# Kernel tuning notes

Measured on AMD Instinct MI355X. Metric: run time of the kernel, lower is better.

## Reference

```python
import jax, jax.numpy as jnp
import numpy as np

NUM_HEADS = 2

def mha(q, k, v, w_in, b_in, w_out, b_out):
    # torch nn.MultiheadAttention with batch_first=True, packed in_proj
    E = q.shape[-1]
    Dh = E // NUM_HEADS
    wq, wk, wv = jnp.split(w_in, 3, axis=0)
    bq, bk, bv = jnp.split(b_in, 3, axis=0)
    qh = (q @ wq.T + bq).reshape(q.shape[0], q.shape[1], NUM_HEADS, Dh)
    kh = (k @ wk.T + bk).reshape(k.shape[0], k.shape[1], NUM_HEADS, Dh)
    vh = (v @ wv.T + bv).reshape(v.shape[0], v.shape[1], NUM_HEADS, Dh)
    scores = jnp.einsum('blhd,bmhd->bhlm', qh, kh) / jnp.sqrt(jnp.asarray(Dh, q.dtype))
    attn = jax.nn.softmax(scores, axis=-1)
    ctx = jnp.einsum('bhlm,bmhd->blhd', attn, vh).reshape(q.shape[0], q.shape[1], E)
    return ctx @ w_out.T + b_out


def setup_inputs() -> dict:
    key = jax.random.key(0)
    ks = jax.random.split(key, 10)
    B, S, F, E, H = 16384, 512, 4, 8, 16
    s = 0.3
    return {
        'x': jax.random.normal(ks[0], (B, S, E), jnp.float32),
        'Q': jax.random.normal(ks[1], (F, E), jnp.float32) * s,
        'sa_w_in': jax.random.normal(ks[2], (3 * E, E), jnp.float32) * s,
        'sa_b_in': jnp.zeros((3 * E,), jnp.float32),
        'sa_w_out': jax.random.normal(ks[3], (E, E), jnp.float32) * s,
        'sa_b_out': jnp.zeros((E,), jnp.float32),
        'ca_w_in': jax.random.normal(ks[4], (3 * E, E), jnp.float32) * s,
        'ca_b_in': jnp.zeros((3 * E,), jnp.float32),
        'ca_w_out': jax.random.normal(ks[5], (E, E), jnp.float32) * s,
        'ca_b_out': jnp.zeros((E,), jnp.float32),
        'r_w1': jax.random.normal(ks[6], (H, F * E), jnp.float32) * s,
        'r_b1': jnp.zeros((H,), jnp.float32),
        'r_w2': jax.random.normal(ks[7], (1, H), jnp.float32) * s,
        'r_b2': jnp.zeros((1,), jnp.float32),
    }


def reference(x, Q, sa_w_in, sa_b_in, sa_w_out, sa_b_out,
              ca_w_in, ca_b_in, ca_w_out, ca_b_out,
              r_w1, r_b1, r_w2, r_b2):
    B = x.shape[0]
    # self-attention over the (batch-identical) factor queries
    Qb = jnp.broadcast_to(Q[None], (B,) + Q.shape)  # [B, F, E]
    Q_upd = mha(Qb, Qb, Qb, sa_w_in, sa_b_in, sa_w_out, sa_b_out)
    # cross-attention: factors attend over the input sequence
    Q_cross = mha(Q_upd, x, x, ca_w_in, ca_b_in, ca_w_out, ca_b_out)  # [B, F, E]
    similarity = jnp.einsum('bfe,bse->bfs', Q_cross, x)  # [B, F, S]
    attn_weights = jax.nn.softmax(similarity, axis=-1)
    final_factors = jnp.einsum('bfs,bse->bfe', attn_weights, x)  # [B, F, E]
    fused = final_factors.reshape(B, -1)  # [B, F*E]
    h = jax.nn.relu(fused @ r_w1.T + r_b1)
    out = h @ r_w2.T + r_b2  # [B, 1]
    return out, similarity
```

## Files before the change

kernel.cpp:

```cpp
#include <hip/hip_runtime.h>

#define SEQ 512
#define EMB 8
#define NFAC 4

typedef float v2f __attribute__((ext_vector_type(2)));

__device__ __forceinline__ float rfl(float v) {
    return __int_as_float(__builtin_amdgcn_readfirstlane(__float_as_int(v)));
}

__global__ void precompute_kernel(
    const float* __restrict__ Q,
    const float* __restrict__ sa_w_in, const float* __restrict__ sa_b_in,
    const float* __restrict__ sa_w_out, const float* __restrict__ sa_b_out,
    const float* __restrict__ ca_w_in, const float* __restrict__ ca_b_in,
    const float* __restrict__ ca_w_out, const float* __restrict__ ca_b_out,
    float* __restrict__ ws)
{
    const int t = threadIdx.x;
    __shared__ float sw[608];
    __shared__ float sqh[32], skh[32], svh[32], sctx[32], sQu[32], sqc[32];
    enum { OQ = 0, SWIN = 32, SBIN = 224, SWOUT = 248, SBOUT = 312,
           CWIN = 320, CBIN = 512, CWOUT = 536, CBOUT = 600 };

    for (int i = t; i < 32;  i += 64) sw[OQ + i]    = Q[i];
    for (int i = t; i < 192; i += 64) sw[SWIN + i]  = sa_w_in[i];
    for (int i = t; i < 24;  i += 64) sw[SBIN + i]  = sa_b_in[i];
    for (int i = t; i < 64;  i += 64) sw[SWOUT + i] = sa_w_out[i];
    if (t < 8) sw[SBOUT + t] = sa_b_out[t];
    for (int i = t; i < 192; i += 64) sw[CWIN + i]  = ca_w_in[i];
    for (int i = t; i < 24;  i += 64) sw[CBIN + i]  = ca_b_in[i];
    for (int i = t; i < 64;  i += 64) sw[CWOUT + i] = ca_w_out[i];
    if (t < 8) sw[CBOUT + t] = ca_b_out[t];
    __syncthreads();

    {
        const int e2 = t >> 3, e = t & 7;
        float m0 = 0.f, m1 = 0.f;
        #pragma unroll
        for (int d = 0; d < 4; ++d) {
            m0 += sw[CWOUT + e2 * 8 + d]     * sw[CWIN + (16 + d) * 8 + e];
            m1 += sw[CWOUT + e2 * 8 + 4 + d] * sw[CWIN + (20 + d) * 8 + e];
        }
        ws[72 + t]  = m0;
        ws[136 + t] = m1;
    }
    if (t < 8) {
        float a = sw[CBOUT + t];
        #pragma unroll
        for (int d = 0; d < 8; ++d) a += sw[CWOUT + t * 8 + d] * sw[CBIN + 16 + d];
        ws[200 + t] = a;
    }

    if (t < 32) {
        const int l = t >> 3, j = t & 7;
        float aq = sw[SBIN + j], ak = sw[SBIN + 8 + j], av = sw[SBIN + 16 + j];
        #pragma unroll
        for (int e = 0; e < 8; ++e) {
            const float q = sw[OQ + l * 8 + e];
            aq += q * sw[SWIN + j * 8 + e];
            ak += q * sw[SWIN + (8 + j) * 8 + e];
            av += q * sw[SWIN + (16 + j) * 8 + e];
        }
        sqh[t] = aq; skh[t] = ak; svh[t] = av;
    }
    __syncthreads();

    if (t < 8) {
        const int h = t >> 2, l = t & 3;
        float sc[4], mx = -1e30f;
        #pragma unroll
        for (int m = 0; m < 4; ++m) {
            float a = 0.f;
            #pragma unroll
            for (int d = 0; d < 4; ++d) a += sqh[l * 8 + h * 4 + d] * skh[m * 8 + h * 4 + d];
            sc[m] = 0.5f * a;
            mx = fmaxf(mx, sc[m]);
        }
        float ssum = 0.f;
        #pragma unroll
        for (int m = 0; m < 4; ++m) { sc[m] = __expf(sc[m] - mx); ssum += sc[m]; }
        const float inv = 1.f / ssum;
        #pragma unroll
        for (int d = 0; d < 4; ++d) {
            float a = 0.f;
            #pragma unroll
            for (int m = 0; m < 4; ++m) a += sc[m] * svh[m * 8 + h * 4 + d];
            sctx[l * 8 + h * 4 + d] = a * inv;
        }
    }
    __syncthreads();

    if (t < 32) {
        const int l = t >> 3, e2 = t & 7;
        float a = sw[SBOUT + e2];
        #pragma unroll
        for (int e = 0; e < 8; ++e) a += sctx[l * 8 + e] * sw[SWOUT + e2 * 8 + e];
        sQu[l * 8 + e2] = a;
    }
    __syncthreads();

    if (t < 32) {
        const int l = t >> 3, j = t & 7;
        float a = sw[CBIN + j];
        #pragma unroll
        for (int e = 0; e < 8; ++e) a += sQu[l * 8 + e] * sw[CWIN + j * 8 + e];
        sqc[l * 8 + j] = a;
    }
    __syncthreads();

    {
        const int p = t >> 3, e = t & 7, h = p >> 2, f = p & 3;
        float a = 0.f;
        #pragma unroll
        for (int d = 0; d < 4; ++d)
            a += sqc[f * 8 + h * 4 + d] * sw[CWIN + (8 + h * 4 + d) * 8 + e];
        ws[p * 8 + e] = 0.5f * a;
    }
    if (t < 8) {
        const int p = t, h = p >> 2, f = p & 3;
        float a = 0.f;
        #pragma unroll
        for (int d = 0; d < 4; ++d) a += sqc[f * 8 + h * 4 + d] * sw[CBIN + 8 + h * 4 + d];
        ws[64 + p] = 0.5f * a;
    }
}

__global__ __launch_bounds__(256, 4) void fused_kernel(
    const float* __restrict__ x,
    const float* __restrict__ r_w1, const float* __restrict__ r_b1,
    const float* __restrict__ r_w2, const float* __restrict__ r_b2,
    const float* __restrict__ ws,
    float* __restrict__ out, float* __restrict__ sim_out)
{
    const int b = blockIdx.x;
    const int tid = threadIdx.x;
    const int w = __builtin_amdgcn_readfirstlane(tid >> 6);
    const int lane = tid & 63;
    const int c7 = lane & 7;

    __shared__ float su[64];
    __shared__ float sff[32];

    const float* xb = x + (size_t)b * (SEQ * EMB);

    const int p0 = 2 * w, p1 = 2 * w + 1;
    v2f wq0[4], wq1[4];
    #pragma unroll
    for (int i = 0; i < 4; ++i) {
        wq0[i] = v2f{rfl(ws[p0 * 8 + 2 * i]), rfl(ws[p0 * 8 + 2 * i + 1])};
        wq1[i] = v2f{rfl(ws[p1 * 8 + 2 * i]), rfl(ws[p1 * 8 + 2 * i + 1])};
    }
    const float cb0 = rfl(ws[64 + p0]), cb1 = rfl(ws[64 + p1]);

    float4 L0[8], L1[8];
    #pragma unroll
    for (int j = 0; j < 8; ++j) {
        const float4* xp = (const float4*)(xb + (lane + 64 * j) * 8);
        L0[j] = xp[0];
        L1[j] = xp[1];
    }

    v2f xa0[4] = {}, xa1[4] = {};
    float sum0 = 0.f, sum1 = 0.f;
    #pragma unroll
    for (int j = 0; j < 8; ++j) {
        v2f xv[4];
        xv[0] = v2f{L0[j].x, L0[j].y}; xv[1] = v2f{L0[j].z, L0[j].w};
        xv[2] = v2f{L1[j].x, L1[j].y}; xv[3] = v2f{L1[j].z, L1[j].w};
        v2f s0 = {cb0, 0.f}, s1 = {cb1, 0.f};
        #pragma unroll
        for (int i = 0; i < 4; ++i) { s0 += wq0[i] * xv[i]; s1 += wq1[i] * xv[i]; }
        const float e0 = __expf(s0.x + s0.y), e1 = __expf(s1.x + s1.y);
        sum0 += e0; sum1 += e1;
        #pragma unroll
        for (int i = 0; i < 4; ++i) { xa0[i] += e0 * xv[i]; xa1[i] += e1 * xv[i]; }
    }
    float* a0 = (float*)xa0;
    float* a1 = (float*)xa1;
    #pragma unroll
    for (int m = 1; m < 8; m <<= 1) {
        sum0 += __shfl_xor(sum0, m, 64);
        sum1 += __shfl_xor(sum1, m, 64);
        #pragma unroll
        for (int e = 0; e < 8; ++e) {
            a0[e] += __shfl_xor(a0[e], m, 64);
            a1[e] += __shfl_xor(a1[e], m, 64);
        }
    }
    float v0 = a0[0], v1 = a1[0];
    #pragma unroll
    for (int e = 1; e < 8; ++e) {
        v0 = (c7 == e) ? a0[e] : v0;
        v1 = (c7 == e) ? a1[e] : v1;
    }
    #pragma unroll
    for (int m = 8; m < 64; m <<= 1) {
        sum0 += __shfl_xor(sum0, m, 64);
        sum1 += __shfl_xor(sum1, m, 64);
        v0 += __shfl_xor(v0, m, 64);
        v1 += __shfl_xor(v1, m, 64);
    }
    if (lane < 8) {
        su[p0 * 8 + lane] = v0 / sum0;
        su[p1 * 8 + lane] = v1 / sum1;
    }
    __syncthreads();

    float u0[8], u1[8];
    #pragma unroll
    for (int e = 0; e < 8; ++e) { u0[e] = su[w * 8 + e]; u1[e] = su[32 + w * 8 + e]; }
    float qv = ws[200 + c7];
    #pragma unroll
    for (int e = 0; e < 8; ++e)
        qv += ws[72 + c7 * 8 + e] * u0[e] + ws[136 + c7 * 8 + e] * u1[e];
    v2f qcr[4];
    #pragma unroll
    for (int i = 0; i < 4; ++i)
        qcr[i] = v2f{__shfl(qv, 2 * i, 64), __shfl(qv, 2 * i + 1, 64)};

    v2f fac[4] = {};
    float fsum = 0.f;
    float* simb = sim_out + (size_t)b * (NFAC * SEQ) + w * SEQ;
    #pragma unroll
    for (int j = 0; j < 8; ++j) {
        v2f xv[4];
        xv[0] = v2f{L0[j].x, L0[j].y}; xv[1] = v2f{L0[j].z, L0[j].w};
        xv[2] = v2f{L1[j].x, L1[j].y}; xv[3] = v2f{L1[j].z, L1[j].w};
        v2f sv = qcr[0] * xv[0];
        sv += qcr[1] * xv[1];
        sv += qcr[2] * xv[2];
        sv += qcr[3] * xv[3];
        const float sim = sv.x + sv.y;
        simb[lane + 64 * j] = sim;
        const float ez = __expf(sim);
        fsum += ez;
        #pragma unroll
        for (int i = 0; i < 4; ++i) fac[i] += ez * xv[i];
    }
    float* fa = (float*)fac;
    #pragma unroll
    for (int m = 1; m < 8; m <<= 1) {
        fsum += __shfl_xor(fsum, m, 64);
        #pragma unroll
        for (int e = 0; e < 8; ++e) fa[e] += __shfl_xor(fa[e], m, 64);
    }
    float fv = fa[0];
    #pragma unroll
    for (int e = 1; e < 8; ++e) fv = (c7 == e) ? fa[e] : fv;
    #pragma unroll
    for (int m = 8; m < 64; m <<= 1) {
        fsum += __shfl_xor(fsum, m, 64);
        fv += __shfl_xor(fv, m, 64);
    }
    if (lane < 8) sff[w * 8 + lane] = fv / fsum;
    __syncthreads();

    if (tid < 16) {
        float a = r_b1[tid];
        const float4* w1p = (const float4*)(r_w1 + tid * 32);
        #pragma unroll
        for (int k = 0; k < 8; ++k) {
            float4 ww = w1p[k];
            a += ww.x * sff[4 * k + 0] + ww.y * sff[4 * k + 1]
               + ww.z * sff[4 * k + 2] + ww.w * sff[4 * k + 3];
        }
        a = fmaxf(a, 0.f);
        float v = a * r_w2[tid];
        v += __shfl_xor(v, 1, 64);
        v += __shfl_xor(v, 2, 64);
        v += __shfl_xor(v, 4, 64);
        v += __shfl_xor(v, 8, 64);
        if (tid == 0) out[b] = v + r_b2[0];
    }
}

extern "C" void kernel_launch(void* const* d_in, const int* in_sizes, int n_in,
                              void* d_out, int out_size, void* d_ws, size_t ws_size,
                              hipStream_t stream) {
    const float* x        = (const float*)d_in[0];
    const float* Q        = (const float*)d_in[1];
    const float* sa_w_in  = (const float*)d_in[2];
    const float* sa_b_in  = (const float*)d_in[3];
    const float* sa_w_out = (const float*)d_in[4];
    const float* sa_b_out = (const float*)d_in[5];
    const float* ca_w_in  = (const float*)d_in[6];
    const float* ca_b_in  = (const float*)d_in[7];
    const float* ca_w_out = (const float*)d_in[8];
    const float* ca_b_out = (const float*)d_in[9];
    const float* r_w1     = (const float*)d_in[10];
    const float* r_b1     = (const float*)d_in[11];
    const float* r_w2     = (const float*)d_in[12];
    const float* r_b2     = (const float*)d_in[13];

    float* out = (float*)d_out;
    const int B = in_sizes[0] / (SEQ * EMB);
    float* sim = out + B;
    float* ws  = (float*)d_ws;

    precompute_kernel<<<1, 64, 0, stream>>>(Q, sa_w_in, sa_b_in, sa_w_out, sa_b_out,
                                            ca_w_in, ca_b_in, ca_w_out, ca_b_out, ws);
    fused_kernel<<<B, 256, 0, stream>>>(x, r_w1, r_b1, r_w2, r_b2, ws, out, sim);
}
```

Before: 439.7 us.

## Stage x tile in padded LDS instead of registers and raise occupancy

The kernel now loads each batch's 512x8 input slice into shared memory with coalesced float4 loads, using a padded index to avoid bank conflicts. Both passes read x back from LDS instead of holding 64 floats per thread in registers. This frees registers, so launch bounds are raised to 8 blocks per CU to get more waves in flight to hide global memory latency. In exchange it adds a block barrier, LDS read traffic per pass and about 18KB of LDS per block, which may itself limit occupancy.

Result: no change. 432.9 us (-1.6%).

```diff
diff --git a/kernel.cpp b/kernel.cpp
--- a/kernel.cpp
+++ b/kernel.cpp
@@ -9,6 +9,8 @@
 __device__ __forceinline__ float rfl(float v) {
     return __int_as_float(__builtin_amdgcn_readfirstlane(__float_as_int(v)));
 }
+
+__device__ __forceinline__ int ldsc(int c) { return c + (c >> 3); }
 
 __global__ void precompute_kernel(
     const float* __restrict__ Q,
@@ -127,7 +129,7 @@
     }
 }
 
-__global__ __launch_bounds__(256, 4) void fused_kernel(
+__global__ __launch_bounds__(256, 8) void fused_kernel(
     const float* __restrict__ x,
     const float* __restrict__ r_w1, const float* __restrict__ r_b1,
     const float* __restrict__ r_w2, const float* __restrict__ r_b2,
@@ -140,10 +142,20 @@
     const int lane = tid & 63;
     const int c7 = lane & 7;
 
+    __shared__ float4 sx[1152];
     __shared__ float su[64];
     __shared__ float sff[32];
 
     const float* xb = x + (size_t)b * (SEQ * EMB);
+
+    {
+        const float4* xg = (const float4*)xb;
+        #pragma unroll
+        for (int i = 0; i < 4; ++i) {
+            const int c = tid + 256 * i;
+            sx[ldsc(c)] = xg[c];
+        }
+    }
 
     const int p0 = 2 * w, p1 = 2 * w + 1;
     v2f wq0[4], wq1[4];
@@ -153,22 +165,18 @@
         wq1[i] = v2f{rfl(ws[p1 * 8 + 2 * i]), rfl(ws[p1 * 8 + 2 * i + 1])};
     }
     const float cb0 = rfl(ws[64 + p0]), cb1 = rfl(ws[64 + p1]);
-
-    float4 L0[8], L1[8];
-    #pragma unroll
-    for (int j = 0; j < 8; ++j) {
-        const float4* xp = (const float4*)(xb + (lane + 64 * j) * 8);
-        L0[j] = xp[0];
-        L1[j] = xp[1];
-    }
+    __syncthreads();
 
     v2f xa0[4] = {}, xa1[4] = {};
     float sum0 = 0.f, sum1 = 0.f;
     #pragma unroll
     for (int j = 0; j < 8; ++j) {
+        const int s = lane + 64 * j;
+        const float4 lo = sx[ldsc(2 * s)];
+        const float4 hi = sx[ldsc(2 * s + 1)];
         v2f xv[4];
-        xv[0] = v2f{L0[j].x, L0[j].y}; xv[1] = v2f{L0[j].z, L0[j].w};
-        xv[2] = v2f{L1[j].x, L1[j].y}; xv[3] = v2f{L1[j].z, L1[j].w};
+        xv[0] = v2f{lo.x, lo.y}; xv[1] = v2f{lo.z, lo.w};
+        xv[2] = v2f{hi.x, hi.y}; xv[3] = v2f{hi.z, hi.w};
         v2f s0 = {cb0, 0.f}, s1 = {cb1, 0.f};
         #pragma unroll
         for (int i = 0; i < 4; ++i) { s0 += wq0[i] * xv[i]; s1 += wq1[i] * xv[i]; }
@@ -225,15 +233,18 @@
     float* simb = sim_out + (size_t)b * (NFAC * SEQ) + w * SEQ;
     #pragma unroll
     for (int j = 0; j < 8; ++j) {
+        const int s = lane + 64 * j;
+        const float4 lo = sx[ldsc(2 * s)];
+        const float4 hi = sx[ldsc(2 * s + 1)];
         v2f xv[4];
-        xv[0] = v2f{L0[j].x, L0[j].y}; xv[1] = v2f{L0[j].z, L0[j].w};
-        xv[2] = v2f{L1[j].x, L1[j].y}; xv[3] = v2f{L1[j].z, L1[j].w};
+        xv[0] = v2f{lo.x, lo.y}; xv[1] = v2f{lo.z, lo.w};
+        xv[2] = v2f{hi.x, hi.y}; xv[3] = v2f{hi.z, hi.w};
         v2f sv = qcr[0] * xv[0];
         sv += qcr[1] * xv[1];
         sv += qcr[2] * xv[2];
         sv += qcr[3] * xv[3];
         const float sim = sv.x + sv.y;
-        simb[lane + 64 * j] = sim;
+        simb[s] = sim;
         const float ez = __expf(sim);
         fsum += ez;
         #pragma unroll
```
